# Optimization experiments

Measured on AMD Instinct MI355X. Metric: run time of the kernel, lower is better.

The kernel has to match this reference:

```python
import jax, jax.numpy as jnp
import numpy as np

NUM_EXPERTS = 16
HALF = NUM_EXPERTS // 2


def setup_inputs() -> dict:
    key = jax.random.key(0)
    ks = jax.random.split(key, 10)
    B, D_IN, D_HID, D_OUT = 4096, 1024, 2048, 1024
    s1 = 1.0 / np.sqrt(D_IN)
    s2 = 1.0 / np.sqrt(D_HID)
    return {
        "x": jax.random.normal(ks[0], (B, D_IN), jnp.float32),
        "y": jax.random.normal(ks[1], (B, D_IN), jnp.float32),
        "z": jax.random.normal(ks[2], (B, D_IN), jnp.float32),
        "W1": jax.random.normal(ks[3], (NUM_EXPERTS, D_IN, D_HID), jnp.float32) * s1,
        "b1": jax.random.normal(ks[4], (NUM_EXPERTS, D_HID), jnp.float32) * s1,
        "W2": jax.random.normal(ks[5], (NUM_EXPERTS, D_HID, D_OUT), jnp.float32) * s2,
        "b2": jax.random.normal(ks[6], (NUM_EXPERTS, D_OUT), jnp.float32) * s2,
        "Wg1": jax.random.normal(ks[7], (D_IN, HALF), jnp.float32),
        "Wg2": jax.random.normal(ks[8], (D_IN, HALF), jnp.float32),
        "Wg3": jax.random.normal(ks[9], (D_IN, HALF), jnp.float32),
    }


def _experts(inp, W1, b1, W2, b2):
    # all experts on one input as a single batched GEMM pair (dropout is identity in eval)
    h = jax.nn.relu(jnp.einsum('bi,eih->ebh', inp, W1) + b1[:, None, :])
    return jnp.einsum('ebh,eho->ebo', h, W2) + b2[:, None, :]  # [E, B, O]


def _channel(inp, W1, b1, W2, b2, Wg):
    # Original samples num_experts/2 experts at random; deterministic reference
    # uses the first half (same math, fixed selection).
    eo = _experts(inp, W1, b1, W2, b2)[:HALF]          # [E/2, B, O]
    gates = jax.nn.softmax(inp @ Wg, axis=1)           # [B, E/2]
    return jnp.einsum('be,ebo->bo', gates, eo)         # [B, O]


def reference(x, y, z, W1, b1, W2, b2, Wg1, Wg2, Wg3):
    o1 = _channel(x, W1, b1, W2, b2, Wg1)
    o2 = _channel(y, W1, b1, W2, b2, Wg2)
    o3 = _channel(z, W1, b1, W2, b2, Wg3)
    return jnp.concatenate([o1, o2, o3], axis=1)
```

## Files before the change

kernel.cpp:

```cpp
#include <hip/hip_runtime.h>
#include <hip/hip_fp16.h>
#include <stdint.h>

#define B_ROWS 4096
#define D_IN   1024
#define D_HID  2048
#define D_OUT  1024
#define NEXP   8
#define NCH    3
#define MTOT   (B_ROWS * NCH)

typedef _Float16 f16;
typedef __attribute__((ext_vector_type(4))) _Float16 f16x4;
typedef __attribute__((ext_vector_type(8))) _Float16 f16x8;
typedef __attribute__((ext_vector_type(4))) float f32x4;

typedef __attribute__((address_space(1))) const void gvoid_t;
typedef __attribute__((address_space(3))) void lvoid_t;

__device__ __forceinline__ void glds16(const void* g, void* l) {
  __builtin_amdgcn_global_load_lds((gvoid_t*)g, (lvoid_t*)l, 16, 0, 0);
}

__global__ __launch_bounds__(256) void gates_kernel(
    const float* __restrict__ x, const float* __restrict__ y, const float* __restrict__ z,
    const float* __restrict__ Wg1, const float* __restrict__ Wg2, const float* __restrict__ Wg3,
    float* __restrict__ gates) {
  int wave = blockIdx.x * 4 + (threadIdx.x >> 6);
  int lane = threadIdx.x & 63;
  int c = wave >> 12;
  int b = wave & 4095;
  const float* inp = (c == 0) ? x : (c == 1) ? y : z;
  const float* Wg  = (c == 0) ? Wg1 : (c == 1) ? Wg2 : Wg3;
  const float* row = inp + (size_t)b * D_IN;
  float acc[8];
#pragma unroll
  for (int e = 0; e < 8; ++e) acc[e] = 0.f;
  for (int k = lane; k < D_IN; k += 64) {
    float xv = row[k];
    const float* w = Wg + (size_t)k * 8;
#pragma unroll
    for (int e = 0; e < 8; ++e) acc[e] += xv * w[e];
  }
#pragma unroll
  for (int off = 32; off > 0; off >>= 1) {
#pragma unroll
    for (int e = 0; e < 8; ++e) acc[e] += __shfl_xor(acc[e], off, 64);
  }
  if (lane == 0) {
    float m = acc[0];
#pragma unroll
    for (int e = 1; e < 8; ++e) m = fmaxf(m, acc[e]);
    float s = 0.f, ex[8];
#pragma unroll
    for (int e = 0; e < 8; ++e) { ex[e] = expf(acc[e] - m); s += ex[e]; }
    float inv = 1.f / s;
    float* go = gates + (size_t)(c * B_ROWS + b) * 8;
#pragma unroll
    for (int e = 0; e < 8; ++e) go[e] = ex[e] * inv;
  }
}

__global__ __launch_bounds__(256) void conv_inp(const float* __restrict__ in,
                                                f16* __restrict__ o) {
  int i = (blockIdx.x * 256 + threadIdx.x) * 4;
  float4 v = *(const float4*)(in + i);
  f16x4 p = {(f16)v.x, (f16)v.y, (f16)v.z, (f16)v.w};
  *(f16x4*)(o + i) = p;
}

__global__ __launch_bounds__(256) void conv_transpose(const float* __restrict__ W,
                                                      f16* __restrict__ Wt,
                                                      int K, int N) {
  W  += (size_t)blockIdx.z * K * N;
  Wt += (size_t)blockIdx.z * K * N;
  int n0 = blockIdx.x * 64, k0 = blockIdx.y * 64;
  __shared__ f16 t[64][72];
  int tid = threadIdx.x;
  int rr = tid >> 4;
  int cq = (tid & 15) * 4;
#pragma unroll
  for (int it = 0; it < 4; ++it) {
    int r = rr + it * 16;
    float4 v = *(const float4*)(W + (size_t)(k0 + r) * N + n0 + cq);
    t[r][cq + 0] = (f16)v.x; t[r][cq + 1] = (f16)v.y;
    t[r][cq + 2] = (f16)v.z; t[r][cq + 3] = (f16)v.w;
  }
  __syncthreads();
#pragma unroll
  for (int it = 0; it < 2; ++it) {
    int idx = tid + it * 256;
    int nr = idx >> 3;
    int kq = (idx & 7) * 8;
    f16x8 o;
#pragma unroll
    for (int j = 0; j < 8; ++j) o[j] = t[kq + j][nr];
    *(f16x8*)(Wt + (size_t)(n0 + nr) * K + k0 + kq) = o;
  }
}

__global__ __launch_bounds__(256, 2) void gemm1_kernel(
    const f16* __restrict__ A, const f16* __restrict__ Bt,
    const float* __restrict__ b1, const float* __restrict__ gch,
    f16* __restrict__ H, int e0, int hrows) {
  const int K = D_IN, NK = D_IN / 32;
  int ez = blockIdx.z, e = e0 + ez;
  const f16* Be = Bt + (size_t)ez * D_HID * D_IN;
  f16* He = H + (size_t)ez * (size_t)hrows * D_HID;
  int m0 = blockIdx.x * 128, n0 = blockIdx.y * 128;
  int tid = threadIdx.x, wid = tid >> 6, lane = tid & 63;
  int wr = wid >> 1, wc = wid & 1;

  __shared__ __align__(16) f16 sA[2][128 * 32];
  __shared__ __align__(16) f16 sB[2][128 * 32];

  int kq = lane & 3;
  int ra0 = (wid * 2 + 0) * 16 + (lane >> 2);
  int ra1 = (wid * 2 + 1) * 16 + (lane >> 2);
  const f16* gA0 = A  + (size_t)(m0 + ra0) * K + ((kq ^ (ra0 & 3)) * 8);
  const f16* gA1 = A  + (size_t)(m0 + ra1) * K + ((kq ^ (ra1 & 3)) * 8);
  const f16* gB0 = Be + (size_t)(n0 + ra0) * K + ((kq ^ (ra0 & 3)) * 8);
  const f16* gB1 = Be + (size_t)(n0 + ra1) * K + ((kq ^ (ra1 & 3)) * 8);

  f32x4 zz = {0.f, 0.f, 0.f, 0.f};
  f32x4 acc[4][4];
#pragma unroll
  for (int i = 0; i < 4; ++i)
#pragma unroll
    for (int j = 0; j < 4; ++j) acc[i][j] = zz;

  int arow = wr * 64 + (lane & 15);
  int bcol = wc * 64 + (lane & 15);
  int kblk = lane >> 4;
  int aoff = arow * 32 + ((kblk ^ (arow & 3)) * 8);
  int boff = bcol * 32 + ((kblk ^ (bcol & 3)) * 8);

  auto stage = [&](int kt, int buf) {
    int ko = kt * 32;
    glds16(gA0 + ko, &sA[buf][(wid * 2 + 0) * 512]);
    glds16(gA1 + ko, &sA[buf][(wid * 2 + 1) * 512]);
    glds16(gB0 + ko, &sB[buf][(wid * 2 + 0) * 512]);
    glds16(gB1 + ko, &sB[buf][(wid * 2 + 1) * 512]);
  };

  stage(0, 0);
  __syncthreads();
  for (int kt = 0; kt < NK; ++kt) {
    int buf = kt & 1;
    if (kt + 1 < NK) stage(kt + 1, buf ^ 1);
    f16x8 af[4], bf[4];
#pragma unroll
    for (int i = 0; i < 4; ++i) {
      af[i] = *(const f16x8*)&sA[buf][aoff + i * 512];
      bf[i] = *(const f16x8*)&sB[buf][boff + i * 512];
    }
#pragma unroll
    for (int mi = 0; mi < 4; ++mi)
#pragma unroll
      for (int ni = 0; ni < 4; ++ni)
        acc[mi][ni] = __builtin_amdgcn_mfma_f32_16x16x32_f16(af[mi], bf[ni], acc[mi][ni], 0, 0, 0);
    __syncthreads();
  }

  float bv[4];
#pragma unroll
  for (int ni = 0; ni < 4; ++ni)
    bv[ni] = b1[(size_t)e * D_HID + n0 + wc * 64 + ni * 16 + (lane & 15)];
  int colb = n0 + wc * 64 + (lane & 15);
#pragma unroll
  for (int mi = 0; mi < 4; ++mi) {
#pragma unroll
    for (int r = 0; r < 4; ++r) {
      int grow = m0 + wr * 64 + mi * 16 + (lane >> 4) * 4 + r;
      float gv = gch[(size_t)grow * 8 + e];
      f16* hp = He + (size_t)grow * D_HID + colb;
#pragma unroll
      for (int ni = 0; ni < 4; ++ni) {
        float h = acc[mi][ni][r] + bv[ni];
        h = h > 0.f ? h : 0.f;
        hp[ni * 16] = (f16)(h * gv);
      }
    }
  }
}

__global__ __launch_bounds__(256, 2) void gemm2_kernel(
    const f16* __restrict__ H, const f16* __restrict__ Bt,
    const float* __restrict__ b2, const float* __restrict__ gch,
    float* __restrict__ out, int e0, int ge, int cbase, int accflag, int hrows) {
  const int K = D_HID;
  int m0 = blockIdx.x * 128, n0 = blockIdx.y * 128;
  int tid = threadIdx.x, wid = tid >> 6, lane = tid & 63;
  int wr = wid >> 1, wc = wid & 1;

  __shared__ __align__(16) f16 sA[2][128 * 32];
  __shared__ __align__(16) f16 sB[2][128 * 32];

  int kq = lane & 3;
  int ra0 = (wid * 2 + 0) * 16 + (lane >> 2);
  int ra1 = (wid * 2 + 1) * 16 + (lane >> 2);
  size_t oA0 = (size_t)(m0 + ra0) * K + ((kq ^ (ra0 & 3)) * 8);
  size_t oA1 = (size_t)(m0 + ra1) * K + ((kq ^ (ra1 & 3)) * 8);
  size_t oB0 = (size_t)(n0 + ra0) * K + ((kq ^ (ra0 & 3)) * 8);
  size_t oB1 = (size_t)(n0 + ra1) * K + ((kq ^ (ra1 & 3)) * 8);
  const size_t EA = (size_t)hrows * D_HID;
  const size_t EB = (size_t)D_OUT * D_HID;

  f32x4 zz = {0.f, 0.f, 0.f, 0.f};
  f32x4 acc[4][4];
#pragma unroll
  for (int i = 0; i < 4; ++i)
#pragma unroll
    for (int j = 0; j < 4; ++j) acc[i][j] = zz;

  int arow = wr * 64 + (lane & 15);
  int bcol = wc * 64 + (lane & 15);
  int kblk = lane >> 4;
  int aoff = arow * 32 + ((kblk ^ (arow & 3)) * 8);
  int boff = bcol * 32 + ((kblk ^ (bcol & 3)) * 8);

  int S = ge * (K / 32);
  auto stage = [&](int s, int buf) {
    int ee = s >> 6; size_t ko = (size_t)(s & 63) * 32;
    glds16(H  + (size_t)ee * EA + oA0 + ko, &sA[buf][(wid * 2 + 0) * 512]);
    glds16(H  + (size_t)ee * EA + oA1 + ko, &sA[buf][(wid * 2 + 1) * 512]);
    glds16(Bt + (size_t)ee * EB + oB0 + ko, &sB[buf][(wid * 2 + 0) * 512]);
    glds16(Bt + (size_t)ee * EB + oB1 + ko, &sB[buf][(wid * 2 + 1) * 512]);
  };

  stage(0, 0);
  __syncthreads();
  for (int s = 0; s < S; ++s) {
    int buf = s & 1;
    if (s + 1 < S) stage(s + 1, buf ^ 1);
    f16x8 af[4], bf[4];
#pragma unroll
    for (int i = 0; i < 4; ++i) {
      af[i] = *(const f16x8*)&sA[buf][aoff + i * 512];
      bf[i] = *(const f16x8*)&sB[buf][boff + i * 512];
    }
#pragma unroll
    for (int mi = 0; mi < 4; ++mi)
#pragma unroll
      for (int ni = 0; ni < 4; ++ni)
        acc[mi][ni] = __builtin_amdgcn_mfma_f32_16x16x32_f16(af[mi], bf[ni], acc[mi][ni], 0, 0, 0);
    __syncthreads();
  }

  float* sb2 = (float*)&sA[0][0];
  for (int i = tid; i < ge * 128; i += 256)
    sb2[i] = b2[(size_t)(e0 + (i >> 7)) * D_OUT + n0 + (i & 127)];
  __syncthreads();

  int cit = wc * 64 + (lane & 15);
#pragma unroll
  for (int mi = 0; mi < 4; ++mi) {
#pragma unroll
    for (int r = 0; r < 4; ++r) {
      int grow = m0 + wr * 64 + mi * 16 + (lane >> 4) * 4 + r;
      int orow, cb;
      if (cbase < 0) { orow = grow & (B_ROWS - 1); cb = (grow >> 12) * D_OUT; }
      else           { orow = grow;                cb = cbase; }
      const float* gv = gch + (size_t)grow * 8;
      float* po = out + (size_t)orow * (NCH * D_OUT) + cb + n0 + cit;
#pragma unroll
      for (int ni = 0; ni < 4; ++ni) {
        float bias = 0.f;
        for (int ee = 0; ee < ge; ++ee)
          bias += gv[e0 + ee] * sb2[ee * 128 + cit + ni * 16];
        float v = acc[mi][ni][r] + bias;
        if (accflag) po[ni * 16] += v; else po[ni * 16] = v;
      }
    }
  }
}

extern "C" void kernel_launch(void* const* d_in, const int* in_sizes, int n_in,
                              void* d_out, int out_size, void* d_ws, size_t ws_size,
                              hipStream_t stream) {
  const float* x   = (const float*)d_in[0];
  const float* y   = (const float*)d_in[1];
  const float* z   = (const float*)d_in[2];
  const float* W1  = (const float*)d_in[3];
  const float* b1  = (const float*)d_in[4];
  const float* W2  = (const float*)d_in[5];
  const float* b2  = (const float*)d_in[6];
  const float* Wg1 = (const float*)d_in[7];
  const float* Wg2 = (const float*)d_in[8];
  const float* Wg3 = (const float*)d_in[9];
  float* out = (float*)d_out;
  char* ws = (char*)d_ws;

  const size_t MB = (size_t)1 << 20;
  const size_t inpE = (size_t)B_ROWS * D_IN;
  float* gates = (float*)ws;

  hipLaunchKernelGGL(gates_kernel, dim3(NCH * B_ROWS / 4), dim3(256), 0, stream,
                     x, y, z, Wg1, Wg2, Wg3, gates);

  size_t base = (512u << 10) + (size_t)MTOT * D_IN * sizeof(f16);
  size_t perE = 56 * MB;

  if (ws_size >= base + perE) {
    f16* inp16 = (f16*)(ws + (512u << 10));
    int EG = (int)((ws_size - base) / perE);
    if (EG > NEXP) EG = NEXP;
    f16* W1t = (f16*)(ws + base);
    f16* W2t = (f16*)(ws + base + (size_t)EG * (4 * MB));
    f16* Hb  = (f16*)(ws + base + (size_t)EG * (8 * MB));

    hipLaunchKernelGGL(conv_inp, dim3(B_ROWS * D_IN / 1024), dim3(256), 0, stream, x, inp16);
    hipLaunchKernelGGL(conv_inp, dim3(B_ROWS * D_IN / 1024), dim3(256), 0, stream, y, inp16 + inpE);
    hipLaunchKernelGGL(conv_inp, dim3(B_ROWS * D_IN / 1024), dim3(256), 0, stream, z, inp16 + 2 * inpE);

    for (int e0 = 0; e0 < NEXP; e0 += EG) {
      int ge = (EG < NEXP - e0) ? EG : (NEXP - e0);
      hipLaunchKernelGGL(conv_transpose, dim3(D_HID / 64, D_IN / 64, ge), dim3(256), 0, stream,
                         W1 + (size_t)e0 * D_IN * D_HID, W1t, D_IN, D_HID);
      hipLaunchKernelGGL(conv_transpose, dim3(D_OUT / 64, D_HID / 64, ge), dim3(256), 0, stream,
                         W2 + (size_t)e0 * D_HID * D_OUT, W2t, D_HID, D_OUT);
      hipLaunchKernelGGL(gemm1_kernel, dim3(MTOT / 128, 16, ge), dim3(256), 0, stream,
                         inp16, W1t, b1, gates, Hb, e0, MTOT);
      hipLaunchKernelGGL(gemm2_kernel, dim3(MTOT / 128, 8, 1), dim3(256), 0, stream,
                         Hb, W2t, b2, gates, out, e0, ge, -1, e0 > 0 ? 1 : 0, MTOT);
    }
  } else {
    const int CH = 1024;
    f16* inp16 = (f16*)(ws + (512u << 10));
    f16* W1t   = (f16*)(ws + (512u << 10) + 8 * MB);
    f16* W2t   = (f16*)(ws + (512u << 10) + 12 * MB);
    f16* Hb    = (f16*)(ws + (512u << 10) + 16 * MB);

    for (int c = 0; c < NCH; ++c) {
      const float* inp = c == 0 ? x : c == 1 ? y : z;
      const float* gch = gates + (size_t)c * B_ROWS * 8;
      hipLaunchKernelGGL(conv_inp, dim3(B_ROWS * D_IN / 1024), dim3(256), 0, stream, inp, inp16);
      for (int e = 0; e < NEXP; ++e) {
        hipLaunchKernelGGL(conv_transpose, dim3(D_HID / 64, D_IN / 64, 1), dim3(256), 0, stream,
                           W1 + (size_t)e * D_IN * D_HID, W1t, D_IN, D_HID);
        hipLaunchKernelGGL(conv_transpose, dim3(D_OUT / 64, D_HID / 64, 1), dim3(256), 0, stream,
                           W2 + (size_t)e * D_HID * D_OUT, W2t, D_HID, D_OUT);
        for (int mb = 0; mb < B_ROWS; mb += CH) {
          hipLaunchKernelGGL(gemm1_kernel, dim3(CH / 128, 16, 1), dim3(256), 0, stream,
                             inp16 + (size_t)mb * D_IN, W1t, b1, gch + (size_t)mb * 8,
                             Hb, e, CH);
          hipLaunchKernelGGL(gemm2_kernel, dim3(CH / 128, 8, 1), dim3(256), 0, stream,
                             Hb, W2t, b2, gch + (size_t)mb * 8,
                             out + (size_t)mb * (NCH * D_OUT), e, 1, c * D_OUT,
                             e > 0 ? 1 : 0, CH);
        }
      }
    }
  }
}
```

Before: 1.310 ms.

## Split gemm2 expert reduction across grid z with atomic accumulation

The second GEMM's long K loop over all experts is split across two z-slices of the grid. Each slice handles half the experts and accumulates into a pre-zeroed output with atomicAdd, and only slice 0 of the first expert group adds the gated bias. The aim is to double the block count (768 to 1536) and improve occupancy and load balance across CUs. The cost is a zeroing pass over the output, atomic read-modify-write traffic, and nondeterministic float summation order.

After: 1.386 ms. +5.8%, slower.

```diff
diff --git a/kernel.cpp b/kernel.cpp
--- a/kernel.cpp
+++ b/kernel.cpp
@@ -20,6 +20,11 @@
 
 __device__ __forceinline__ void glds16(const void* g, void* l) {
   __builtin_amdgcn_global_load_lds((gvoid_t*)g, (lvoid_t*)l, 16, 0, 0);
+}
+
+__global__ __launch_bounds__(256) void zero_out(float* __restrict__ o) {
+  int i = (blockIdx.x * 256 + threadIdx.x) * 4;
+  *(float4*)(o + i) = float4{0.f, 0.f, 0.f, 0.f};
 }
 
 __global__ __launch_bounds__(256) void gates_kernel(
@@ -187,9 +192,10 @@
 __global__ __launch_bounds__(256, 2) void gemm2_kernel(
     const f16* __restrict__ H, const f16* __restrict__ Bt,
     const float* __restrict__ b2, const float* __restrict__ gch,
-    float* __restrict__ out, int e0, int ge, int cbase, int accflag, int hrows) {
+    float* __restrict__ out, int e0, int espan, int cbase, int addbias, int hrows) {
   const int K = D_HID;
   int m0 = blockIdx.x * 128, n0 = blockIdx.y * 128;
+  int ez0 = blockIdx.z * espan;
   int tid = threadIdx.x, wid = tid >> 6, lane = tid & 63;
   int wr = wid >> 1, wc = wid & 1;
 
@@ -219,9 +225,9 @@
   int aoff = arow * 32 + ((kblk ^ (arow & 3)) * 8);
   int boff = bcol * 32 + ((kblk ^ (bcol & 3)) * 8);
 
-  int S = ge * (K / 32);
+  int S = espan * (K / 32);
   auto stage = [&](int s, int buf) {
-    int ee = s >> 6; size_t ko = (size_t)(s & 63) * 32;
+    int ee = ez0 + (s >> 6); size_t ko = (size_t)(s & 63) * 32;
     glds16(H  + (size_t)ee * EA + oA0 + ko, &sA[buf][(wid * 2 + 0) * 512]);
     glds16(H  + (size_t)ee * EA + oA1 + ko, &sA[buf][(wid * 2 + 1) * 512]);
     glds16(Bt + (size_t)ee * EB + oB0 + ko, &sB[buf][(wid * 2 + 0) * 512]);
@@ -247,10 +253,13 @@
     __syncthreads();
   }
 
+  int dobias = addbias && (blockIdx.z == 0);
   float* sb2 = (float*)&sA[0][0];
-  for (int i = tid; i < ge * 128; i += 256)
-    sb2[i] = b2[(size_t)(e0 + (i >> 7)) * D_OUT + n0 + (i & 127)];
-  __syncthreads();
+  if (dobias) {
+    for (int i = tid; i < NEXP * 128; i += 256)
+      sb2[i] = b2[(size_t)(i >> 7) * D_OUT + n0 + (i & 127)];
+    __syncthreads();
+  }
 
   int cit = wc * 64 + (lane & 15);
 #pragma unroll
@@ -265,11 +274,14 @@
       float* po = out + (size_t)orow * (NCH * D_OUT) + cb + n0 + cit;
 #pragma unroll
       for (int ni = 0; ni < 4; ++ni) {
-        float bias = 0.f;
-        for (int ee = 0; ee < ge; ++ee)
-          bias += gv[e0 + ee] * sb2[ee * 128 + cit + ni * 16];
-        float v = acc[mi][ni][r] + bias;
-        if (accflag) po[ni * 16] += v; else po[ni * 16] = v;
+        float v = acc[mi][ni][r];
+        if (dobias) {
+          float bias = 0.f;
+          for (int ee = 0; ee < NEXP; ++ee)
+            bias += gv[ee] * sb2[ee * 128 + cit + ni * 16];
+          v += bias;
+        }
+        atomicAdd(po + ni * 16, v);
       }
     }
   }
@@ -295,6 +307,7 @@
   const size_t inpE = (size_t)B_ROWS * D_IN;
   float* gates = (float*)ws;
 
+  hipLaunchKernelGGL(zero_out, dim3(out_size / 1024), dim3(256), 0, stream, out);
   hipLaunchKernelGGL(gates_kernel, dim3(NCH * B_ROWS / 4), dim3(256), 0, stream,
                      x, y, z, Wg1, Wg2, Wg3, gates);
 
@@ -321,8 +334,10 @@
                          W2 + (size_t)e0 * D_HID * D_OUT, W2t, D_HID, D_OUT);
       hipLaunchKernelGGL(gemm1_kernel, dim3(MTOT / 128, 16, ge), dim3(256), 0, stream,
                          inp16, W1t, b1, gates, Hb, e0, MTOT);
-      hipLaunchKernelGGL(gemm2_kernel, dim3(MTOT / 128, 8, 1), dim3(256), 0, stream,
-                         Hb, W2t, b2, gates, out, e0, ge, -1, e0 > 0 ? 1 : 0, MTOT);
+      int nsplit = (ge & 1) ? 1 : 2;
+      int espan = ge / nsplit;
+      hipLaunchKernelGGL(gemm2_kernel, dim3(MTOT / 128, 8, nsplit), dim3(256), 0, stream,
+                         Hb, W2t, b2, gates, out, e0, espan, -1, (e0 == 0) ? 1 : 0, MTOT);
     }
   } else {
     const int CH = 1024;
@@ -347,7 +362,7 @@
           hipLaunchKernelGGL(gemm2_kernel, dim3(CH / 128, 8, 1), dim3(256), 0, stream,
                              Hb, W2t, b2, gch + (size_t)mb * 8,
                              out + (size_t)mb * (NCH * D_OUT), e, 1, c * D_OUT,
-                             e > 0 ? 1 : 0, CH);
+                             (e == 0) ? 1 : 0, CH);
         }
       }
     }
```

## Replace expert GEMMs with 256x256-tile, 4-buffer pipelined 512-thread kernels

Applied to the files above, without the earlier changes.

Adds gemm1_big and gemm2_big, which compute 256x256 output tiles with 8 waves, a 4-slot LDS ring with prefetch distance two, split barriers and s_setprio around the MFMA bursts. The larger tiles double operand reuse per LDS load, and the deeper pipeline is meant to hide global-to-LDS latency and cut redundant global traffic. The second-layer bias, summed over all experts, is now folded in once on the first expert group instead of per group. The cost is 128KB of LDS per block, which likely allows only one block per CU, plus higher register pressure from 32 accumulator tiles.

New measurement: 1.542 ms. +17.7%, slower.

```diff
diff --git a/kernel.cpp b/kernel.cpp
--- a/kernel.cpp
+++ b/kernel.cpp
@@ -99,6 +99,240 @@
   }
 }
 
+
+__global__ __launch_bounds__(512, 2) void gemm1_big(
+    const f16* __restrict__ A, const f16* __restrict__ Bt,
+    const float* __restrict__ b1, const float* __restrict__ gch,
+    f16* __restrict__ H, int e0, int hrows) {
+  const int K = D_IN, NT = D_IN / 32;
+  int ez = blockIdx.z, e = e0 + ez;
+  const f16* Be = Bt + (size_t)ez * D_HID * D_IN;
+  f16* He = H + (size_t)ez * (size_t)hrows * D_HID;
+  int m0 = blockIdx.x * 256, n0 = blockIdx.y * 256;
+  int tid = threadIdx.x, wid = tid >> 6, lane = tid & 63;
+  int wr = wid >> 2, wc = wid & 3;
+
+  __shared__ __align__(16) f16 sA[4][256 * 32];
+  __shared__ __align__(16) f16 sB[4][256 * 32];
+
+  int srow = lane >> 2;
+  int scs  = ((lane & 3) ^ ((lane >> 3) & 3)) * 8;
+  int rA0 = (wid * 2 + 0) * 16 + srow;
+  int rA1 = (wid * 2 + 1) * 16 + srow;
+  const f16* gA0 = A  + (size_t)(m0 + rA0) * K + scs;
+  const f16* gA1 = A  + (size_t)(m0 + rA1) * K + scs;
+  const f16* gB0 = Be + (size_t)(n0 + rA0) * K + scs;
+  const f16* gB1 = Be + (size_t)(n0 + rA1) * K + scs;
+  int dA0 = (wid * 2 + 0) * 512;
+  int dA1 = (wid * 2 + 1) * 512;
+
+  int r15 = lane & 15, kb = lane >> 4;
+  int swz = (kb ^ ((r15 >> 1) & 3)) * 8;
+  int abase = (wr * 128 + r15) * 32 + swz;
+  int bbase = (wc * 64  + r15) * 32 + swz;
+
+  f32x4 zz = {0.f, 0.f, 0.f, 0.f};
+  f32x4 acc[8][4];
+#pragma unroll
+  for (int i = 0; i < 8; ++i)
+#pragma unroll
+    for (int j = 0; j < 4; ++j) acc[i][j] = zz;
+
+  glds16(gA0,      &sA[0][dA0]); glds16(gA1,      &sA[0][dA1]);
+  glds16(gB0,      &sB[0][dA0]); glds16(gB1,      &sB[0][dA1]);
+  glds16(gA0 + 32, &sA[1][dA0]); glds16(gA1 + 32, &sA[1][dA1]);
+  glds16(gB0 + 32, &sB[1][dA0]); glds16(gB1 + 32, &sB[1][dA1]);
+  asm volatile("s_waitcnt vmcnt(4)" ::: "memory");
+  __builtin_amdgcn_s_barrier();
+
+  for (int t = 0; t < NT; ++t) {
+    const f16* sAb = sA[t & 3];
+    const f16* sBb = sB[t & 3];
+    int tp = t + 2;
+    f16x8 af[4], bf[4];
+    if (tp < NT) {
+      glds16(gA0 + tp * 32, &sA[tp & 3][dA0]);
+      glds16(gA1 + tp * 32, &sA[tp & 3][dA1]);
+    }
+#pragma unroll
+    for (int i = 0; i < 4; ++i) {
+      af[i] = *(const f16x8*)&sAb[abase + i * 512];
+      bf[i] = *(const f16x8*)&sBb[bbase + i * 512];
+    }
+    __builtin_amdgcn_s_barrier();
+    __builtin_amdgcn_s_setprio(1);
+#pragma unroll
+    for (int mi = 0; mi < 4; ++mi)
+#pragma unroll
+      for (int ni = 0; ni < 4; ++ni)
+        acc[mi][ni] = __builtin_amdgcn_mfma_f32_16x16x32_f16(af[mi], bf[ni], acc[mi][ni], 0, 0, 0);
+    __builtin_amdgcn_s_setprio(0);
+    __builtin_amdgcn_s_barrier();
+    if (tp < NT) {
+      glds16(gB0 + tp * 32, &sB[tp & 3][dA0]);
+      glds16(gB1 + tp * 32, &sB[tp & 3][dA1]);
+    }
+#pragma unroll
+    for (int i = 0; i < 4; ++i)
+      af[i] = *(const f16x8*)&sAb[abase + (i + 4) * 512];
+    __builtin_amdgcn_s_barrier();
+    __builtin_amdgcn_s_setprio(1);
+#pragma unroll
+    for (int mi = 0; mi < 4; ++mi)
+#pragma unroll
+      for (int ni = 0; ni < 4; ++ni)
+        acc[mi + 4][ni] = __builtin_amdgcn_mfma_f32_16x16x32_f16(af[mi], bf[ni], acc[mi + 4][ni], 0, 0, 0);
+    __builtin_amdgcn_s_setprio(0);
+    if (tp < NT) asm volatile("s_waitcnt vmcnt(4)" ::: "memory");
+    else         asm volatile("s_waitcnt vmcnt(0)" ::: "memory");
+    __builtin_amdgcn_s_barrier();
+  }
+
+  float bv[4];
+#pragma unroll
+  for (int ni = 0; ni < 4; ++ni)
+    bv[ni] = b1[(size_t)e * D_HID + n0 + wc * 64 + ni * 16 + (lane & 15)];
+  int colb = n0 + wc * 64 + (lane & 15);
+#pragma unroll
+  for (int mi = 0; mi < 8; ++mi) {
+#pragma unroll
+    for (int r = 0; r < 4; ++r) {
+      int grow = m0 + wr * 128 + mi * 16 + (lane >> 4) * 4 + r;
+      float gv = gch[(size_t)grow * 8 + e];
+      f16* hp = He + (size_t)grow * D_HID + colb;
+#pragma unroll
+      for (int ni = 0; ni < 4; ++ni) {
+        float h = acc[mi][ni][r] + bv[ni];
+        h = h > 0.f ? h : 0.f;
+        hp[ni * 16] = (f16)(h * gv);
+      }
+    }
+  }
+}
+
+__global__ __launch_bounds__(512, 2) void gemm2_big(
+    const f16* __restrict__ H, const f16* __restrict__ Bt,
+    const float* __restrict__ b2, const float* __restrict__ gch,
+    float* __restrict__ out, int ge, int addbias, int accflag, int hrows) {
+  const int NT = 0 + ge * (D_HID / 32);
+  int m0 = blockIdx.x * 256, n0 = blockIdx.y * 256;
+  int tid = threadIdx.x, wid = tid >> 6, lane = tid & 63;
+  int wr = wid >> 2, wc = wid & 3;
+  const size_t EA = (size_t)hrows * D_HID;
+  const size_t EB = (size_t)D_OUT * D_HID;
+
+  __shared__ __align__(16) f16 sA[4][256 * 32];
+  __shared__ __align__(16) f16 sB[4][256 * 32];
+
+  int srow = lane >> 2;
+  int scs  = ((lane & 3) ^ ((lane >> 3) & 3)) * 8;
+  int rA0 = (wid * 2 + 0) * 16 + srow;
+  int rA1 = (wid * 2 + 1) * 16 + srow;
+  const f16* gA0 = H  + (size_t)(m0 + rA0) * D_HID + scs;
+  const f16* gA1 = H  + (size_t)(m0 + rA1) * D_HID + scs;
+  const f16* gB0 = Bt + (size_t)(n0 + rA0) * D_HID + scs;
+  const f16* gB1 = Bt + (size_t)(n0 + rA1) * D_HID + scs;
+  int dA0 = (wid * 2 + 0) * 512;
+  int dA1 = (wid * 2 + 1) * 512;
+
+  int r15 = lane & 15, kb = lane >> 4;
+  int swz = (kb ^ ((r15 >> 1) & 3)) * 8;
+  int abase = (wr * 128 + r15) * 32 + swz;
+  int bbase = (wc * 64  + r15) * 32 + swz;
+
+  f32x4 zz = {0.f, 0.f, 0.f, 0.f};
+  f32x4 acc[8][4];
+#pragma unroll
+  for (int i = 0; i < 8; ++i)
+#pragma unroll
+    for (int j = 0; j < 4; ++j) acc[i][j] = zz;
+
+  glds16(gA0,      &sA[0][dA0]); glds16(gA1,      &sA[0][dA1]);
+  glds16(gB0,      &sB[0][dA0]); glds16(gB1,      &sB[0][dA1]);
+  glds16(gA0 + 32, &sA[1][dA0]); glds16(gA1 + 32, &sA[1][dA1]);
+  glds16(gB0 + 32, &sB[1][dA0]); glds16(gB1 + 32, &sB[1][dA1]);
+  asm volatile("s_waitcnt vmcnt(4)" ::: "memory");
+  __builtin_amdgcn_s_barrier();
+
+  for (int t = 0; t < NT; ++t) {
+    const f16* sAb = sA[t & 3];
+    const f16* sBb = sB[t & 3];
+    int tp = t + 2;
+    size_t po = 0;
+    if (tp < NT) po = (size_t)(tp >> 6) * EA + (size_t)(tp & 63) * 32;
+    size_t pb = 0;
+    if (tp < NT) pb = (size_t)(tp >> 6) * EB + (size_t)(tp & 63) * 32;
+    f16x8 af[4], bf[4];
+    if (tp < NT) {
+      glds16(gA0 + po, &sA[tp & 3][dA0]);
+      glds16(gA1 + po, &sA[tp & 3][dA1]);
+    }
+#pragma unroll
+    for (int i = 0; i < 4; ++i) {
+      af[i] = *(const f16x8*)&sAb[abase + i * 512];
+      bf[i] = *(const f16x8*)&sBb[bbase + i * 512];
+    }
+    __builtin_amdgcn_s_barrier();
+    __builtin_amdgcn_s_setprio(1);
+#pragma unroll
+    for (int mi = 0; mi < 4; ++mi)
+#pragma unroll
+      for (int ni = 0; ni < 4; ++ni)
+        acc[mi][ni] = __builtin_amdgcn_mfma_f32_16x16x32_f16(af[mi], bf[ni], acc[mi][ni], 0, 0, 0);
+    __builtin_amdgcn_s_setprio(0);
+    __builtin_amdgcn_s_barrier();
+    if (tp < NT) {
+      glds16(gB0 + pb, &sB[tp & 3][dA0]);
+      glds16(gB1 + pb, &sB[tp & 3][dA1]);
+    }
+#pragma unroll
+    for (int i = 0; i < 4; ++i)
+      af[i] = *(const f16x8*)&sAb[abase + (i + 4) * 512];
+    __builtin_amdgcn_s_barrier();
+    __builtin_amdgcn_s_setprio(1);
+#pragma unroll
+    for (int mi = 0; mi < 4; ++mi)
+#pragma unroll
+      for (int ni = 0; ni < 4; ++ni)
+        acc[mi + 4][ni] = __builtin_amdgcn_mfma_f32_16x16x32_f16(af[mi], bf[ni], acc[mi + 4][ni], 0, 0, 0);
+    __builtin_amdgcn_s_setprio(0);
+    if (tp < NT) asm volatile("s_waitcnt vmcnt(4)" ::: "memory");
+    else         asm volatile("s_waitcnt vmcnt(0)" ::: "memory");
+    __builtin_amdgcn_s_barrier();
+  }
+
+  float* sb2 = (float*)&sA[0][0];
+  if (addbias) {
+    for (int i = tid; i < NEXP * 256; i += 512)
+      sb2[i] = b2[(size_t)(i >> 8) * D_OUT + n0 + (i & 255)];
+    __syncthreads();
+  }
+
+  int cit = wc * 64 + (lane & 15);
+#pragma unroll
+  for (int mi = 0; mi < 8; ++mi) {
+#pragma unroll
+    for (int r = 0; r < 4; ++r) {
+      int grow = m0 + wr * 128 + mi * 16 + (lane >> 4) * 4 + r;
+      int orow = grow & (B_ROWS - 1);
+      int cb = (grow >> 12) * D_OUT;
+      const float* gv = gch + (size_t)grow * 8;
+      float* po2 = out + (size_t)orow * (NCH * D_OUT) + cb + n0 + cit;
+#pragma unroll
+      for (int ni = 0; ni < 4; ++ni) {
+        float v = acc[mi][ni][r];
+        if (addbias) {
+          float bias = 0.f;
+          for (int ee = 0; ee < NEXP; ++ee)
+            bias += gv[ee] * sb2[ee * 256 + cit + ni * 16];
+          v += bias;
+        }
+        if (accflag) po2[ni * 16] += v; else po2[ni * 16] = v;
+      }
+    }
+  }
+}
+
 __global__ __launch_bounds__(256, 2) void gemm1_kernel(
     const f16* __restrict__ A, const f16* __restrict__ Bt,
     const float* __restrict__ b1, const float* __restrict__ gch,
@@ -110,10 +344,8 @@
   int m0 = blockIdx.x * 128, n0 = blockIdx.y * 128;
   int tid = threadIdx.x, wid = tid >> 6, lane = tid & 63;
   int wr = wid >> 1, wc = wid & 1;
-
   __shared__ __align__(16) f16 sA[2][128 * 32];
   __shared__ __align__(16) f16 sB[2][128 * 32];
-
   int kq = lane & 3;
   int ra0 = (wid * 2 + 0) * 16 + (lane >> 2);
   int ra1 = (wid * 2 + 1) * 16 + (lane >> 2);
@@ -121,20 +353,17 @@
   const f16* gA1 = A  + (size_t)(m0 + ra1) * K + ((kq ^ (ra1 & 3)) * 8);
   const f16* gB0 = Be + (size_t)(n0 + ra0) * K + ((kq ^ (ra0 & 3)) * 8);
   const f16* gB1 = Be + (size_t)(n0 + ra1) * K + ((kq ^ (ra1 & 3)) * 8);
-
   f32x4 zz = {0.f, 0.f, 0.f, 0.f};
   f32x4 acc[4][4];
 #pragma unroll
   for (int i = 0; i < 4; ++i)
 #pragma unroll
     for (int j = 0; j < 4; ++j) acc[i][j] = zz;
-
   int arow = wr * 64 + (lane & 15);
   int bcol = wc * 64 + (lane & 15);
   int kblk = lane >> 4;
   int aoff = arow * 32 + ((kblk ^ (arow & 3)) * 8);
   int boff = bcol * 32 + ((kblk ^ (bcol & 3)) * 8);
-
   auto stage = [&](int kt, int buf) {
     int ko = kt * 32;
     glds16(gA0 + ko, &sA[buf][(wid * 2 + 0) * 512]);
@@ -142,7 +371,6 @@
     glds16(gB0 + ko, &sB[buf][(wid * 2 + 0) * 512]);
     glds16(gB1 + ko, &sB[buf][(wid * 2 + 1) * 512]);
   };
-
   stage(0, 0);
   __syncthreads();
   for (int kt = 0; kt < NK; ++kt) {
@@ -161,7 +389,6 @@
         acc[mi][ni] = __builtin_amdgcn_mfma_f32_16x16x32_f16(af[mi], bf[ni], acc[mi][ni], 0, 0, 0);
     __syncthreads();
   }
-
   float bv[4];
 #pragma unroll
   for (int ni = 0; ni < 4; ++ni)
@@ -192,10 +419,8 @@
   int m0 = blockIdx.x * 128, n0 = blockIdx.y * 128;
   int tid = threadIdx.x, wid = tid >> 6, lane = tid & 63;
   int wr = wid >> 1, wc = wid & 1;
-
   __shared__ __align__(16) f16 sA[2][128 * 32];
   __shared__ __align__(16) f16 sB[2][128 * 32];
-
   int kq = lane & 3;
   int ra0 = (wid * 2 + 0) * 16 + (lane >> 2);
   int ra1 = (wid * 2 + 1) * 16 + (lane >> 2);
@@ -205,20 +430,17 @@
   size_t oB1 = (size_t)(n0 + ra1) * K + ((kq ^ (ra1 & 3)) * 8);
   const size_t EA = (size_t)hrows * D_HID;
   const size_t EB = (size_t)D_OUT * D_HID;
-
   f32x4 zz = {0.f, 0.f, 0.f, 0.f};
   f32x4 acc[4][4];
 #pragma unroll
   for (int i = 0; i < 4; ++i)
 #pragma unroll
     for (int j = 0; j < 4; ++j) acc[i][j] = zz;
-
   int arow = wr * 64 + (lane & 15);
   int bcol = wc * 64 + (lane & 15);
   int kblk = lane >> 4;
   int aoff = arow * 32 + ((kblk ^ (arow & 3)) * 8);
   int boff = bcol * 32 + ((kblk ^ (bcol & 3)) * 8);
-
   int S = ge * (K / 32);
   auto stage = [&](int s, int buf) {
     int ee = s >> 6; size_t ko = (size_t)(s & 63) * 32;
@@ -227,7 +449,6 @@
     glds16(Bt + (size_t)ee * EB + oB0 + ko, &sB[buf][(wid * 2 + 0) * 512]);
     glds16(Bt + (size_t)ee * EB + oB1 + ko, &sB[buf][(wid * 2 + 1) * 512]);
   };
-
   stage(0, 0);
   __syncthreads();
   for (int s = 0; s < S; ++s) {
@@ -246,12 +467,10 @@
         acc[mi][ni] = __builtin_amdgcn_mfma_f32_16x16x32_f16(af[mi], bf[ni], acc[mi][ni], 0, 0, 0);
     __syncthreads();
   }
-
   float* sb2 = (float*)&sA[0][0];
   for (int i = tid; i < ge * 128; i += 256)
-    sb2[i] = b2[(size_t)(e0 + (i >> 7)) * D_OUT + n0 + (i & 127)];
+    sb2[i] = b2[(size_t)((i >> 7)) * D_OUT + n0 + (i & 127)];
   __syncthreads();
-
   int cit = wc * 64 + (lane & 15);
 #pragma unroll
   for (int mi = 0; mi < 4; ++mi) {
@@ -267,7 +486,7 @@
       for (int ni = 0; ni < 4; ++ni) {
         float bias = 0.f;
         for (int ee = 0; ee < ge; ++ee)
-          bias += gv[e0 + ee] * sb2[ee * 128 + cit + ni * 16];
+          bias += gv[ee] * sb2[ee * 128 + cit + ni * 16];
         float v = acc[mi][ni][r] + bias;
         if (accflag) po[ni * 16] += v; else po[ni * 16] = v;
       }
@@ -319,10 +538,10 @@
                          W1 + (size_t)e0 * D_IN * D_HID, W1t, D_IN, D_HID);
       hipLaunchKernelGGL(conv_transpose, dim3(D_OUT / 64, D_HID / 64, ge), dim3(256), 0, stream,
                          W2 + (size_t)e0 * D_HID * D_OUT, W2t, D_HID, D_OUT);
-      hipLaunchKernelGGL(gemm1_kernel, dim3(MTOT / 128, 16, ge), dim3(256), 0, stream,
+      hipLaunchKernelGGL(gemm1_big, dim3(MTOT / 256, D_HID / 256, ge), dim3(512), 0, stream,
                          inp16, W1t, b1, gates, Hb, e0, MTOT);
-      hipLaunchKernelGGL(gemm2_kernel, dim3(MTOT / 128, 8, 1), dim3(256), 0, stream,
-                         Hb, W2t, b2, gates, out, e0, ge, -1, e0 > 0 ? 1 : 0, MTOT);
+      hipLaunchKernelGGL(gemm2_big, dim3(MTOT / 256, D_OUT / 256), dim3(512), 0, stream,
+                         Hb, W2t, b2, gates, out, ge, (e0 == 0) ? 1 : 0, (e0 > 0) ? 1 : 0, MTOT);
     }
   } else {
     const int CH = 1024;
```
